# Kernel optimization log

Measured on AMD Instinct MI355X. Metric: run time of the kernel, lower is better.

The kernel has to match this reference:

```python
import jax, jax.numpy as jnp
import numpy as np


def _unfold(x, r):
    # x: [b, ch, h, w] -> [b, ch, k*k, h, w], zero-padded 3x3-style neighborhoods
    b, ch, h, w = x.shape
    k = 2 * r + 1
    xp = jnp.pad(x, ((0, 0), (0, 0), (r, r), (r, r)))
    patches = [xp[:, :, i:i + h, j:j + w] for i in range(k) for j in range(k)]
    return jnp.stack(patches, axis=2)


def setup_inputs() -> dict:
    key = jax.random.key(0)
    ks = jax.random.split(key, 6)
    b, c, h, w = 4, 128, 128, 128
    scale = 1.0 / np.sqrt(c)
    return {
        "feature0": jax.random.normal(ks[0], (b, c, h, w), jnp.float32),
        "flow": jax.random.normal(ks[1], (b, 2, h, w), jnp.float32),
        "q_w": jax.random.normal(ks[2], (c, c), jnp.float32) * scale,
        "q_b": jax.random.normal(ks[3], (c,), jnp.float32) * 0.01,
        "k_w": jax.random.normal(ks[4], (c, c), jnp.float32) * scale,
        "k_b": jax.random.normal(ks[5], (c,), jnp.float32) * 0.01,
        "local_window_attn": 1,
        "local_window_radius": 1,
    }


def reference(feature0, flow, q_w, q_b, k_w, k_b, local_window_attn, local_window_radius):
    b, c, h, w = feature0.shape
    inv_sqrt_c = 1.0 / jnp.sqrt(jnp.asarray(c, feature0.dtype))
    x = feature0.reshape(b, c, h * w).transpose(0, 2, 1)  # [b, hw, c]
    q = x @ q_w.T + q_b  # q_proj
    if local_window_attn:
        r = local_window_radius
        kf = x @ k_w.T + k_b  # k_proj applied to original feature
        kmap = kf.transpose(0, 2, 1).reshape(b, c, h, w)
        kwin = _unfold(kmap, r)      # [b, c, k2, h, w]
        fwin = _unfold(flow, r)      # [b, 2, k2, h, w]
        qmap = q.reshape(b, h, w, c)
        scores = jnp.einsum('bhwc,bckhw->bhwk', qmap, kwin) * inv_sqrt_c
        prob = jax.nn.softmax(scores, axis=-1)
        out = jnp.einsum('bhwk,bfkhw->bfhw', prob, fwin)  # [b, 2, h, w]
        return out
    else:
        # NOTE: faithful to source, key = k_proj(q_proj(x))
        key_ = q @ k_w.T + k_b
        value = flow.reshape(b, flow.shape[1], h * w).transpose(0, 2, 1)  # [b, hw, 2]
        scores = jnp.einsum('bnc,bmc->bnm', q, key_) * inv_sqrt_c
        prob = jax.nn.softmax(scores, axis=-1)
        out = jnp.einsum('bnm,bmf->bnf', prob, value)
        return out.reshape(b, h, w, value.shape[-1]).transpose(0, 3, 1, 2)
```

## Files before the change

### kernel.cpp

```cpp
#include <hip/hip_runtime.h>


#define HW 16384
#define NB 4
#define TOT (NB * HW)

__global__ void prep_kernel(const float* __restrict__ qw, const float* __restrict__ qb,
                            const float* __restrict__ kw, const float* __restrict__ kb,
                            float* __restrict__ Mt, float* __restrict__ u,
                            float* __restrict__ v, float* __restrict__ dptr) {
    __shared__ float sa[128];
    __shared__ float red[128];
    int bid = blockIdx.x, tid = threadIdx.x;
    if (bid < 128) {
        int ci = bid;
        if (tid < 128) sa[tid] = qw[tid * 128 + ci];
        __syncthreads();
        int col = tid & 127, h = tid >> 7;
        const float* kwp = kw + (size_t)h * 64 * 128 + col;
        float acc = 0.f;
#pragma unroll 8
        for (int j = 0; j < 64; ++j)
            acc += sa[h * 64 + j] * kwp[(size_t)j * 128];
        if (h) red[col] = acc;
        __syncthreads();
        if (!h) Mt[col * 128 + ci] = acc + red[col];
    } else if (bid == 128) {
        if (tid < 128) sa[tid] = kb[tid];
        __syncthreads();
        if (tid < 128) {
            float acc = 0.f;
#pragma unroll 8
            for (int co = 0; co < 128; ++co) acc += qw[co * 128 + tid] * sa[co];
            u[tid] = acc;
            red[tid] = qb[tid] * sa[tid];
        }
        __syncthreads();
        if (tid == 0) {
            float dd = 0.f;
            for (int i = 0; i < 128; ++i) dd += red[i];
            *dptr = dd;
        }
    } else {
        if (tid < 128) sa[tid] = qb[tid];
        __syncthreads();
        if (tid < 128) {
            float acc = 0.f;
#pragma unroll 8
            for (int co = 0; co < 128; ++co) acc += kw[co * 128 + tid] * sa[co];
            v[tid] = acc;
        }
    }
}

__global__ __launch_bounds__(256, 4)
void proj_kernel(const float* __restrict__ feat, const float* __restrict__ Mt,
                 const float* __restrict__ u, const float* __restrict__ v,
                 const float* __restrict__ dptr, float* __restrict__ y,
                 float* __restrict__ gam, float* __restrict__ del) {
    __shared__ float F[128][64];
    __shared__ float gred[4][64], dred[4][64];

    int tid = threadIdx.x;
    int blk = blockIdx.x;
    int b = blk >> 8, pt = blk & 255;
    int p0 = pt * 64;
    const float* Fb = feat + (size_t)b * 128 * HW + p0;

#pragma unroll
    for (int k = 0; k < 8; ++k) {
        int idx = tid + 256 * k;
        int c = idx >> 4, q = idx & 15;
        *(float4*)&F[c][q * 4] = *(const float4*)(Fb + (size_t)c * HW + q * 4);
    }
    __syncthreads();

    int lane = tid & 63;
    {
        int cq = tid >> 6;
        float g = 0.f, dd = 0.f;
#pragma unroll 8
        for (int j = 0; j < 32; ++j) {
            float xv = F[cq * 32 + j][lane];
            g += xv * u[cq * 32 + j];
            dd += xv * v[cq * 32 + j];
        }
        gred[cq][lane] = g;
        dred[cq][lane] = dd;
    }
    __syncthreads();
    if (tid < 64) {
        float g = gred[0][tid] + gred[1][tid] + gred[2][tid] + gred[3][tid];
        float dd = dred[0][tid] + dred[1][tid] + dred[2][tid] + dred[3][tid] + *dptr;
        gam[(size_t)b * HW + p0 + tid] = g;
        del[(size_t)b * HW + p0 + tid] = dd;
    }

    int wci = __builtin_amdgcn_readfirstlane((tid >> 6) * 32);
    const float* __restrict__ mrow = Mt + wci;
    float acc[32];
#pragma unroll
    for (int i = 0; i < 32; ++i) acc[i] = 0.f;
#pragma unroll 2
    for (int c = 0; c < 128; ++c) {
        float xv = F[c][lane];
#pragma unroll
        for (int i = 0; i < 32; ++i)
            acc[i] = fmaf(mrow[c * 128 + i], xv, acc[i]);
    }
    float* yp = y + ((size_t)b * 128 + wci) * HW + p0 + lane;
#pragma unroll
    for (int i = 0; i < 32; ++i) yp[(size_t)i * HW] = acc[i];
}

__global__ __launch_bounds__(256, 8)
void attn_partial_kernel(const float* __restrict__ feat, const float* __restrict__ y,
                         float* __restrict__ ps) {
    int tid = threadIdx.x;
    int blk = blockIdx.x;
    int cg = blk >> 7;
    int pp = (blk & 127) * 256 + tid;
    int P = pp * 2;
    int b = P >> 14;
    int p = P & (HW - 1);
    const float* xb = feat + ((size_t)b * 128 + cg * 32) * HW + p;
    const float* yb = y + ((size_t)b * 128 + cg * 32) * HW + p;

    float s0[9], s1[9];
#pragma unroll
    for (int k = 0; k < 9; ++k) { s0[k] = 0.f; s1[k] = 0.f; }

#pragma unroll 2
    for (int c = 0; c < 32; ++c) {
        float2 xv = *(const float2*)(xb + (size_t)c * HW);
        const float* yc = yb + (size_t)c * HW;
#pragma unroll
        for (int dy = 0; dy < 3; ++dy) {
            const float* yr = yc + (dy - 1) * 128;
            float2 a  = *(const float2*)(yr - 2);
            float2 bb = *(const float2*)(yr);
            float2 cc = *(const float2*)(yr + 2);
            s0[dy * 3 + 0] += xv.x * a.y;   s1[dy * 3 + 0] += xv.y * bb.x;
            s0[dy * 3 + 1] += xv.x * bb.x;  s1[dy * 3 + 1] += xv.y * bb.y;
            s0[dy * 3 + 2] += xv.x * bb.y;  s1[dy * 3 + 2] += xv.y * cc.x;
        }
    }
    float* pso = ps + (size_t)cg * 9 * TOT + P;
#pragma unroll
    for (int k = 0; k < 9; ++k)
        *(float2*)(pso + (size_t)k * TOT) = make_float2(s0[k], s1[k]);
}

__global__ __launch_bounds__(256, 8)
void attn_final_kernel(const float* __restrict__ flow, const float* __restrict__ ps,
                       const float* __restrict__ gam, const float* __restrict__ del,
                       float* __restrict__ out) {
    int P = blockIdx.x * 256 + threadIdx.x;
    int b = P >> 14, p = P & (HW - 1);
    int row = p >> 7, col = p & 127;
    const float inv = 0.08838834764831845f;

    float g = gam[P];
    float sc[9];
    float mx = -1e30f;
#pragma unroll
    for (int k = 0; k < 9; ++k) {
        int dy = k / 3 - 1, dx = (k % 3) - 1;
        bool valid = ((unsigned)(row + dy) < 128u) && ((unsigned)(col + dx) < 128u);
        float ssum = 0.f;
#pragma unroll
        for (int cg = 0; cg < 4; ++cg) ssum += ps[(size_t)(cg * 9 + k) * TOT + P];
        int nidx = P + dy * 128 + dx;
        nidx = max(0, min(TOT - 1, nidx));
        float s = valid ? (ssum + g + del[nidx]) * inv : 0.f;
        sc[k] = s;
        mx = fmaxf(mx, s);
    }
    float e[9], sum = 0.f;
#pragma unroll
    for (int k = 0; k < 9; ++k) { e[k] = __expf(sc[k] - mx); sum += e[k]; }
    float rs = 1.f / sum;

    float o0 = 0.f, o1 = 0.f;
#pragma unroll
    for (int k = 0; k < 9; ++k) {
        int dy = k / 3 - 1, dx = (k % 3) - 1;
        bool valid = ((unsigned)(row + dy) < 128u) && ((unsigned)(col + dx) < 128u);
        float pr = valid ? e[k] * rs : 0.f;
        int fi0 = b * 2 * HW + p + dy * 128 + dx;
        fi0 = max(0, min(2 * TOT - 1, fi0));
        int fi1 = (b * 2 + 1) * HW + p + dy * 128 + dx;
        fi1 = max(0, min(2 * TOT - 1, fi1));
        o0 += pr * flow[fi0];
        o1 += pr * flow[fi1];
    }
    out[(size_t)(b * 2) * HW + p] = o0;
    out[(size_t)(b * 2 + 1) * HW + p] = o1;
}

extern "C" void kernel_launch(void* const* d_in, const int* in_sizes, int n_in,
                              void* d_out, int out_size, void* d_ws, size_t ws_size,
                              hipStream_t stream) {
    const float* feat = (const float*)d_in[0];
    const float* flow = (const float*)d_in[1];
    const float* qw = (const float*)d_in[2];
    const float* qb = (const float*)d_in[3];
    const float* kw = (const float*)d_in[4];
    const float* kb = (const float*)d_in[5];

    float* ws = (float*)d_ws;
    float* Mt = ws;
    float* u = ws + 16384;
    float* v = ws + 16512;
    float* dptr = ws + 16640;
    float* y = ws + 16896;
    float* gam = y + (size_t)NB * 128 * HW;
    float* del = gam + (size_t)TOT;
    float* ps = del + (size_t)TOT;
    float* out = (float*)d_out;

    prep_kernel<<<130, 256, 0, stream>>>(qw, qb, kw, kb, Mt, u, v, dptr);
    proj_kernel<<<NB * 256, 256, 0, stream>>>(feat, Mt, u, v, dptr, y, gam, del);
    attn_partial_kernel<<<512, 256, 0, stream>>>(feat, y, ps);
    attn_final_kernel<<<256, 256, 0, stream>>>(flow, ps, gam, del, out);
}
```

Measured before the change: 135.2 us.

## Use split-bf16 MFMA for projection and move gamma/delta reductions into partial kernel

The projection GEMM moves from scalar FP32 FMAs over an LDS tile to bf16 MFMA instructions. Both operands are split into high and low bf16 parts and combined with three MFMAs to keep roughly FP32 accuracy. The per-pixel gamma/delta dot products move out of the projection kernel into the attention partial kernel as per-channel-group partial sums, which the final kernel adds up. The prep kernel is also reorganised into fewer, wider blocks. The cost is extra partial-sum memory traffic and bf16 split rounding error.

```diff
diff --git a/kernel.cpp b/kernel.cpp
--- a/kernel.cpp
+++ b/kernel.cpp
@@ -5,117 +5,130 @@
 #define NB 4
 #define TOT (NB * HW)
 
+typedef short bf16x8 __attribute__((ext_vector_type(8)));
+typedef float f32x4 __attribute__((ext_vector_type(4)));
+
+__device__ __forceinline__ unsigned short f2bf(float f) {
+    unsigned u = __float_as_uint(f);
+    return (unsigned short)((u + 0x7fffu + ((u >> 16) & 1u)) >> 16);
+}
+__device__ __forceinline__ float bf2f(unsigned short s) {
+    return __uint_as_float(((unsigned)s) << 16);
+}
+
 __global__ void prep_kernel(const float* __restrict__ qw, const float* __restrict__ qb,
                             const float* __restrict__ kw, const float* __restrict__ kb,
-                            float* __restrict__ Mt, float* __restrict__ u,
-                            float* __restrict__ v, float* __restrict__ dptr) {
-    __shared__ float sa[128];
+                            unsigned short* __restrict__ Mh, unsigned short* __restrict__ Ml,
+                            float* __restrict__ u, float* __restrict__ v,
+                            float* __restrict__ dptr) {
     __shared__ float red[128];
     int bid = blockIdx.x, tid = threadIdx.x;
-    if (bid < 128) {
-        int ci = bid;
-        if (tid < 128) sa[tid] = qw[tid * 128 + ci];
-        __syncthreads();
-        int col = tid & 127, h = tid >> 7;
-        const float* kwp = kw + (size_t)h * 64 * 128 + col;
+    if (bid < 16) {
+        int ci = bid * 8 + (tid >> 5);
+        int cj = (tid & 31) * 4;
+        float4 acc = make_float4(0.f, 0.f, 0.f, 0.f);
+#pragma unroll 4
+        for (int co = 0; co < 128; ++co) {
+            float qv = qw[co * 128 + ci];
+            float4 kv = *(const float4*)(kw + co * 128 + cj);
+            acc.x += qv * kv.x; acc.y += qv * kv.y;
+            acc.z += qv * kv.z; acc.w += qv * kv.w;
+        }
+        int o = ci * 128 + cj;
+        float a[4] = {acc.x, acc.y, acc.z, acc.w};
+#pragma unroll
+        for (int j = 0; j < 4; ++j) {
+            unsigned short h = f2bf(a[j]);
+            Mh[o + j] = h;
+            Ml[o + j] = f2bf(a[j] - bf2f(h));
+        }
+    } else {
+        int half = tid >> 7, t = tid & 127;
+        const float* w  = half ? kw : qw;
+        const float* bv = half ? qb : kb;
         float acc = 0.f;
-#pragma unroll 8
-        for (int j = 0; j < 64; ++j)
-            acc += sa[h * 64 + j] * kwp[(size_t)j * 128];
-        if (h) red[col] = acc;
-        __syncthreads();
-        if (!h) Mt[col * 128 + ci] = acc + red[col];
-    } else if (bid == 128) {
-        if (tid < 128) sa[tid] = kb[tid];
-        __syncthreads();
-        if (tid < 128) {
-            float acc = 0.f;
-#pragma unroll 8
-            for (int co = 0; co < 128; ++co) acc += qw[co * 128 + tid] * sa[co];
-            u[tid] = acc;
-            red[tid] = qb[tid] * sa[tid];
-        }
+#pragma unroll 4
+        for (int co = 0; co < 128; ++co) acc += w[co * 128 + t] * bv[co];
+        if (half) v[t] = acc; else u[t] = acc;
+        if (!half) red[t] = qb[t] * kb[t];
         __syncthreads();
         if (tid == 0) {
             float dd = 0.f;
             for (int i = 0; i < 128; ++i) dd += red[i];
             *dptr = dd;
         }
-    } else {
-        if (tid < 128) sa[tid] = qb[tid];
-        __syncthreads();
-        if (tid < 128) {
-            float acc = 0.f;
-#pragma unroll 8
-            for (int co = 0; co < 128; ++co) acc += kw[co * 128 + tid] * sa[co];
-            v[tid] = acc;
-        }
-    }
+    }
+}
+
+__global__ __launch_bounds__(256, 2)
+void proj_kernel(const float* __restrict__ feat, const unsigned short* __restrict__ MhG,
+                 const unsigned short* __restrict__ MlG, float* __restrict__ y) {
+    int tid = threadIdx.x;
+    int W = blockIdx.x * 4 + (tid >> 6);
+    int lane = tid & 63;
+    int cig = W & 3, pxg = W >> 2;
+    int ci0 = cig * 32;
+    int P0 = pxg * 64;
+    int b = P0 >> 14, p0 = P0 & (HW - 1);
+    int m = lane & 15, q = lane >> 4;
+    const float* xbase = feat + (size_t)b * 128 * HW + p0;
+
+    f32x4 zero = {0.f, 0.f, 0.f, 0.f};
+    f32x4 acc[2][4];
+#pragma unroll
+    for (int t = 0; t < 2; ++t)
+#pragma unroll
+        for (int s = 0; s < 4; ++s) acc[t][s] = zero;
+
+#pragma unroll
+    for (int kc = 0; kc < 4; ++kc) {
+        int c0 = kc * 32;
+        bf16x8 ah[2], al[2];
+#pragma unroll
+        for (int t = 0; t < 2; ++t) {
+            int roff = (ci0 + t * 16 + m) * 128 + c0 + q * 8;
+            ah[t] = *(const bf16x8*)(MhG + roff);
+            al[t] = *(const bf16x8*)(MlG + roff);
+        }
+        bf16x8 bh[4], bl[4];
+#pragma unroll
+        for (int s = 0; s < 4; ++s) {
+            const float* xp = xbase + (size_t)(c0 + q * 8) * HW + s * 16 + m;
+            float xv[8];
+#pragma unroll
+            for (int j = 0; j < 8; ++j) xv[j] = xp[(size_t)j * HW];
+#pragma unroll
+            for (int j = 0; j < 8; ++j) {
+                unsigned short h = f2bf(xv[j]);
+                bh[s][j] = (short)h;
+                bl[s][j] = (short)f2bf(xv[j] - bf2f(h));
+            }
+        }
+#pragma unroll
+        for (int t = 0; t < 2; ++t)
+#pragma unroll
+            for (int s = 0; s < 4; ++s) {
+                acc[t][s] = __builtin_amdgcn_mfma_f32_16x16x32_bf16(ah[t], bh[s], acc[t][s], 0, 0, 0);
+                acc[t][s] = __builtin_amdgcn_mfma_f32_16x16x32_bf16(ah[t], bl[s], acc[t][s], 0, 0, 0);
+                acc[t][s] = __builtin_amdgcn_mfma_f32_16x16x32_bf16(al[t], bh[s], acc[t][s], 0, 0, 0);
+            }
+    }
+
+    int rg = lane >> 4, col = lane & 15;
+#pragma unroll
+    for (int t = 0; t < 2; ++t)
+#pragma unroll
+        for (int s = 0; s < 4; ++s) {
+            float* yp = y + ((size_t)b * 128 + ci0 + t * 16 + rg * 4) * HW + p0 + s * 16 + col;
+#pragma unroll
+            for (int r = 0; r < 4; ++r) yp[(size_t)r * HW] = acc[t][s][r];
+        }
 }
 
 __global__ __launch_bounds__(256, 4)
-void proj_kernel(const float* __restrict__ feat, const float* __restrict__ Mt,
-                 const float* __restrict__ u, const float* __restrict__ v,
-                 const float* __restrict__ dptr, float* __restrict__ y,
-                 float* __restrict__ gam, float* __restrict__ del) {
-    __shared__ float F[128][64];
-    __shared__ float gred[4][64], dred[4][64];
-
-    int tid = threadIdx.x;
-    int blk = blockIdx.x;
-    int b = blk >> 8, pt = blk & 255;
-    int p0 = pt * 64;
-    const float* Fb = feat + (size_t)b * 128 * HW + p0;
-
-#pragma unroll
-    for (int k = 0; k < 8; ++k) {
-        int idx = tid + 256 * k;
-        int c = idx >> 4, q = idx & 15;
-        *(float4*)&F[c][q * 4] = *(const float4*)(Fb + (size_t)c * HW + q * 4);
-    }
-    __syncthreads();
-
-    int lane = tid & 63;
-    {
-        int cq = tid >> 6;
-        float g = 0.f, dd = 0.f;
-#pragma unroll 8
-        for (int j = 0; j < 32; ++j) {
-            float xv = F[cq * 32 + j][lane];
-            g += xv * u[cq * 32 + j];
-            dd += xv * v[cq * 32 + j];
-        }
-        gred[cq][lane] = g;
-        dred[cq][lane] = dd;
-    }
-    __syncthreads();
-    if (tid < 64) {
-        float g = gred[0][tid] + gred[1][tid] + gred[2][tid] + gred[3][tid];
-        float dd = dred[0][tid] + dred[1][tid] + dred[2][tid] + dred[3][tid] + *dptr;
-        gam[(size_t)b * HW + p0 + tid] = g;
-        del[(size_t)b * HW + p0 + tid] = dd;
-    }
-
-    int wci = __builtin_amdgcn_readfirstlane((tid >> 6) * 32);
-    const float* __restrict__ mrow = Mt + wci;
-    float acc[32];
-#pragma unroll
-    for (int i = 0; i < 32; ++i) acc[i] = 0.f;
-#pragma unroll 2
-    for (int c = 0; c < 128; ++c) {
-        float xv = F[c][lane];
-#pragma unroll
-        for (int i = 0; i < 32; ++i)
-            acc[i] = fmaf(mrow[c * 128 + i], xv, acc[i]);
-    }
-    float* yp = y + ((size_t)b * 128 + wci) * HW + p0 + lane;
-#pragma unroll
-    for (int i = 0; i < 32; ++i) yp[(size_t)i * HW] = acc[i];
-}
-
-__global__ __launch_bounds__(256, 8)
 void attn_partial_kernel(const float* __restrict__ feat, const float* __restrict__ y,
-                         float* __restrict__ ps) {
+                         const float* __restrict__ u, const float* __restrict__ v,
+                         float* __restrict__ ps, float* __restrict__ gd) {
     int tid = threadIdx.x;
     int blk = blockIdx.x;
     int cg = blk >> 7;
@@ -129,10 +142,14 @@
     float s0[9], s1[9];
 #pragma unroll
     for (int k = 0; k < 9; ++k) { s0[k] = 0.f; s1[k] = 0.f; }
+    float g0 = 0.f, g1 = 0.f, d0 = 0.f, d1 = 0.f;
 
 #pragma unroll 2
     for (int c = 0; c < 32; ++c) {
         float2 xv = *(const float2*)(xb + (size_t)c * HW);
+        float uc = u[cg * 32 + c], vc = v[cg * 32 + c];
+        g0 += xv.x * uc; g1 += xv.y * uc;
+        d0 += xv.x * vc; d1 += xv.y * vc;
         const float* yc = yb + (size_t)c * HW;
 #pragma unroll
         for (int dy = 0; dy < 3; ++dy) {
@@ -149,18 +166,24 @@
 #pragma unroll
     for (int k = 0; k < 9; ++k)
         *(float2*)(pso + (size_t)k * TOT) = make_float2(s0[k], s1[k]);
-}
-
-__global__ __launch_bounds__(256, 8)
+    *(float2*)(gd + (size_t)(cg * 2 + 0) * TOT + P) = make_float2(g0, g1);
+    *(float2*)(gd + (size_t)(cg * 2 + 1) * TOT + P) = make_float2(d0, d1);
+}
+
+__global__ __launch_bounds__(256, 4)
 void attn_final_kernel(const float* __restrict__ flow, const float* __restrict__ ps,
-                       const float* __restrict__ gam, const float* __restrict__ del,
+                       const float* __restrict__ gd, const float* __restrict__ dptr,
                        float* __restrict__ out) {
     int P = blockIdx.x * 256 + threadIdx.x;
     int b = P >> 14, p = P & (HW - 1);
     int row = p >> 7, col = p & 127;
     const float inv = 0.08838834764831845f;
-
-    float g = gam[P];
+    float dconst = *dptr;
+
+    float g = 0.f;
+#pragma unroll
+    for (int cg = 0; cg < 4; ++cg) g += gd[(size_t)(cg * 2) * TOT + P];
+
     float sc[9];
     float mx = -1e30f;
 #pragma unroll
@@ -170,9 +193,12 @@
         float ssum = 0.f;
 #pragma unroll
         for (int cg = 0; cg < 4; ++cg) ssum += ps[(size_t)(cg * 9 + k) * TOT + P];
-        int nidx = P + dy * 128 + dx;
-        nidx = max(0, min(TOT - 1, nidx));
-        float s = valid ? (ssum + g + del[nidx]) * inv : 0.f;
+        int Pn = P + dy * 128 + dx;
+        Pn = max(0, min(TOT - 1, Pn));
+        float dsum = dconst;
+#pragma unroll
+        for (int cg = 0; cg < 4; ++cg) dsum += gd[(size_t)(cg * 2 + 1) * TOT + Pn];
+        float s = valid ? (ssum + g + dsum) * inv : 0.f;
         sc[k] = s;
         mx = fmaxf(mx, s);
     }
@@ -209,18 +235,18 @@
     const float* kb = (const float*)d_in[5];
 
     float* ws = (float*)d_ws;
-    float* Mt = ws;
-    float* u = ws + 16384;
-    float* v = ws + 16512;
-    float* dptr = ws + 16640;
+    float* u = ws;
+    float* v = ws + 128;
+    float* dptr = ws + 256;
+    unsigned short* Mh = (unsigned short*)(ws + 512);
+    unsigned short* Ml = (unsigned short*)(ws + 8704);
     float* y = ws + 16896;
-    float* gam = y + (size_t)NB * 128 * HW;
-    float* del = gam + (size_t)TOT;
-    float* ps = del + (size_t)TOT;
+    float* ps = ws + 8405760;
+    float* gd = ws + 10765056;
     float* out = (float*)d_out;
 
-    prep_kernel<<<130, 256, 0, stream>>>(qw, qb, kw, kb, Mt, u, v, dptr);
-    proj_kernel<<<NB * 256, 256, 0, stream>>>(feat, Mt, u, v, dptr, y, gam, del);
-    attn_partial_kernel<<<512, 256, 0, stream>>>(feat, y, ps);
-    attn_final_kernel<<<256, 256, 0, stream>>>(flow, ps, gam, del, out);
-}
+    prep_kernel<<<17, 256, 0, stream>>>(qw, qb, kw, kb, Mh, Ml, u, v, dptr);
+    proj_kernel<<<1024, 256, 0, stream>>>(feat, Mh, Ml, y);
+    attn_partial_kernel<<<512, 256, 0, stream>>>(feat, y, u, v, ps, gd);
+    attn_final_kernel<<<256, 256, 0, stream>>>(flow, ps, gd, dptr, out);
+}
```

After: 127.4 us (median of 2 runs). -5.8%, faster.
